# Kernel tuning notes

Measured on AMD Instinct MI355X. Metric: run time of the kernel, lower is better.

Reference implementation:

```python
import jax, jax.numpy as jnp
import numpy as np

B, C, D, H, W = 2, 96, 32, 64, 64
K = 2            # MRConv stride
EPS = 1e-5
SLOPE = 0.2      # LeakyReLU negative slope used by ViG act_layer('leakyrelu')


def conv1x1(x, w, b):
    # 1x1x1 Conv3d == per-voxel channel GEMM. x: [B,Ci,D,H,W], w: [Co,Ci]
    return jnp.einsum('bcdhw,oc->bodhw', x, w) + b[None, :, None, None, None]


def batchnorm(x, g, b):
    # training-mode BatchNorm3d: stats over (B, D, H, W)
    m = x.mean(axis=(0, 2, 3, 4), keepdims=True)
    v = x.var(axis=(0, 2, 3, 4), keepdims=True)
    return (x - m) * jax.lax.rsqrt(v + EPS) * g[None, :, None, None, None] + b[None, :, None, None, None]


def instnorm(x, g, b):
    # InstanceNorm3d: stats over (D, H, W) per sample/channel
    m = x.mean(axis=(2, 3, 4), keepdims=True)
    v = x.var(axis=(2, 3, 4), keepdims=True)
    return (x - m) * jax.lax.rsqrt(v + EPS) * g[None, :, None, None, None] + b[None, :, None, None, None]


def lrelu(x):
    return jnp.where(x >= 0, x, SLOPE * x)


def mr_aggregate(x):
    # MRConv shift/subtract/max, in closed form.
    # Original: x_j = max over axes a, shifts s in range(K, L_a, K) of (x - roll(x, s, a)), init 0.
    # Since shifts cover ALL nonzero multiples of K mod L_a (L_a % K == 0), the rolled values at a
    # position are exactly the other members of its residue class mod K along that axis, and
    # max(0, x - min_excluding_self) == x - min_including_self.  Hence:
    #   x_j = x - min over axes of (strided residue-class min along that axis).
    def axmin(x, axis):
        L = x.shape[axis]
        shp = list(x.shape)
        grp = shp[:axis] + [L // K, K] + shp[axis + 1:]
        xg = x.reshape(grp)
        m = xg.min(axis=axis, keepdims=True)             # min over same residue class
        return jnp.broadcast_to(m, grp).reshape(shp)
    m = jnp.minimum(jnp.minimum(axmin(x, 2), axmin(x, 3)), axmin(x, 4))
    return x - m


def setup_inputs() -> dict:
    key = jax.random.key(0)
    ks = jax.random.split(key, 8)
    f32 = jnp.float32
    def w(k, co, ci):
        return (jax.random.normal(k, (co, ci), dtype=f32) / np.sqrt(ci)).astype(f32)
    return {
        'x': jax.random.normal(ks[0], (B, C, D, H, W), dtype=f32),
        'w_fc1': w(ks[1], C, C), 'b_fc1': jnp.zeros((C,), f32),
        'g_bn1': jnp.ones((C,), f32), 'be_bn1': jnp.zeros((C,), f32),
        'w_g': w(ks[2], 2 * C, 2 * C), 'b_g': jnp.zeros((2 * C,), f32),
        'g_in': jnp.ones((2 * C,), f32), 'be_in': jnp.zeros((2 * C,), f32),
        'w_fc2': w(ks[3], C, 2 * C), 'b_fc2': jnp.zeros((C,), f32),
        'g_bn2': jnp.ones((C,), f32), 'be_bn2': jnp.zeros((C,), f32),
        'w_f1': w(ks[4], 4 * C, C), 'b_f1': jnp.zeros((4 * C,), f32),
        'g_bnf1': jnp.ones((4 * C,), f32), 'be_bnf1': jnp.zeros((4 * C,), f32),
        'w_f2': w(ks[5], C, 4 * C), 'b_f2': jnp.zeros((C,), f32),
        'g_bnf2': jnp.ones((C,), f32), 'be_bnf2': jnp.zeros((C,), f32),
    }


def reference(x, w_fc1, b_fc1, g_bn1, be_bn1, w_g, b_g, g_in, be_in,
              w_fc2, b_fc2, g_bn2, be_bn2, w_f1, b_f1, g_bnf1, be_bnf1,
              w_f2, b_f2, g_bnf2, be_bnf2):
    # ---- Grapher ----
    shortcut = x
    h = batchnorm(conv1x1(x, w_fc1, b_fc1), g_bn1, be_bn1)          # fc1: Conv+BN
    xj = mr_aggregate(h)                                            # MRConv shift-max agg
    hc = jnp.concatenate([h, xj], axis=1)                           # [B,2C,D,H,W]
    hg = lrelu(instnorm(conv1x1(hc, w_g, b_g), g_in, be_in))        # BasicConv: Conv+IN+LeakyReLU
    h = batchnorm(conv1x1(hg, w_fc2, b_fc2), g_bn2, be_bn2)         # fc2: Conv+BN
    x = h + shortcut
    # ---- FFN ----
    shortcut = x
    h = batchnorm(conv1x1(x, w_f1, b_f1), g_bnf1, be_bnf1)
    h = lrelu(h)
    h = batchnorm(conv1x1(h, w_f2, b_f2), g_bnf2, be_bnf2)
    return h + shortcut
```

## Files before the change

kernel.cpp:

```cpp
#include <hip/hip_runtime.h>
#include <hip/hip_bf16.h>


typedef __hip_bfloat16 bf16;
typedef __attribute__((ext_vector_type(8))) short short8;
typedef __attribute__((ext_vector_type(4))) float f4;
typedef __attribute__((ext_vector_type(2))) unsigned uint2v;

#define DEV static __device__ __forceinline__

constexpr int Sq  = 131072;
constexpr int NVq = 262144;

DEV float bu2f(unsigned short u) { return __uint_as_float(((unsigned)u) << 16); }
DEV unsigned short f2bu(float f) {
    unsigned i = __float_as_uint(f);
    unsigned r = i + 0x7FFFu + ((i >> 16) & 1u);
    return (unsigned short)(r >> 16);
}
DEV unsigned cvtpk(float a, float b) {
    unsigned r;
    asm("v_cvt_pk_bf16_f32 %0, %1, %2" : "=v"(r) : "v"(a), "v"(b));
    return r;
}
DEV void glds16(const void* g, void* l) {
    __builtin_amdgcn_global_load_lds(
        (const __attribute__((address_space(1))) unsigned*)g,
        (__attribute__((address_space(3))) unsigned*)l, 16, 0, 0);
}

template<int CIRB, int KP, int CO, int BN, int AMODE, bool PERB>
__global__ __launch_bounds__(256)
void conv_k(const char* __restrict__ A0, const char* __restrict__ A1,
            const char* __restrict__ Wb, const float* __restrict__ bias,
            const float* __restrict__ cfA, const float* __restrict__ cfB,
            bf16* __restrict__ Y, float* __restrict__ part)
{
    constexpr int NSTEP = KP / 64;
    constexpr int NF = BN / 16;
    constexpr int BI = BN / 8;
    __shared__ __align__(16) char smem[16384 + BN * 128];
    char* As = smem;
    char* Bs = smem + 16384;

    const int tid = threadIdx.x;
    const int lane = tid & 63, wid = tid >> 6, l16 = lane & 15, lhi = lane >> 4;
    const int gm = blockIdx.x, gy = blockIdx.y;
    const int v0 = gm * 128;
    const int b = gm >> 10;
    const int n0g = gy * BN;

    f4 acc[2][NF];
#pragma unroll
    for (int nf = 0; nf < NF; ++nf) {
        float bb = bias[n0g + nf * 16 + l16];
        f4 t = {bb, bb, bb, bb};
        acc[0][nf] = t; acc[1][nf] = t;
    }

    for (int s = 0; s < NSTEP; ++s) {
        for (int i = wid; i < BI; i += 4) {
            int o = i * 8 + (lane >> 3);
            glds16(Wb + (size_t)(n0g + o) * (KP * 2) + s * 128 + (((lane & 7) ^ (o & 7)) << 4),
                   Bs + i * 1024);
        }
        if constexpr (AMODE == 0) {
            for (int i = wid; i < 16; i += 4) {
                int r = i * 8 + (lane >> 3);
                glds16(A0 + (size_t)(v0 + r) * CIRB + s * 128 + (((lane & 7) ^ (r & 7)) << 4),
                       As + i * 1024);
            }
        } else {
#pragma unroll
            for (int j = 0; j < 4; ++j) {
                int idx = tid + 256 * j;
                int v = idx >> 3, u = idx & 7;
                int k8 = s * 8 + u;
                short8 hh;
                if constexpr (AMODE == 2) {
                    short8 raw = *(const short8*)(A0 + (size_t)(v0 + v) * CIRB + k8 * 16);
                    int cb = b * KP + k8 * 8;
                    f4 a0 = *(const f4*)(cfA + cb), a1 = *(const f4*)(cfA + cb + 4);
                    f4 d0 = *(const f4*)(cfB + cb), d1 = *(const f4*)(cfB + cb + 4);
#pragma unroll
                    for (int e = 0; e < 4; ++e) {
                        float t0 = fmaf(a0[e], bu2f((unsigned short)raw[e]),     d0[e]);
                        float t1 = fmaf(a1[e], bu2f((unsigned short)raw[e + 4]), d1[e]);
                        t0 = fmaxf(t0, 0.2f * t0);
                        t1 = fmaxf(t1, 0.2f * t1);
                        hh[e] = (short)f2bu(t0); hh[e + 4] = (short)f2bu(t1);
                    }
                } else {
                    if (k8 < 12) {
                        short8 raw = *(const short8*)(A0 + (size_t)(v0 + v) * 192 + k8 * 16);
                        int cb = k8 * 8;
                        f4 a0 = *(const f4*)(cfA + cb), a1 = *(const f4*)(cfA + cb + 4);
                        f4 d0 = *(const f4*)(cfB + cb), d1 = *(const f4*)(cfB + cb + 4);
#pragma unroll
                        for (int e = 0; e < 4; ++e) {
                            hh[e]     = (short)f2bu(fmaf(a0[e], bu2f((unsigned short)raw[e]),     d0[e]));
                            hh[e + 4] = (short)f2bu(fmaf(a1[e], bu2f((unsigned short)raw[e + 4]), d1[e]));
                        }
                    } else {
                        hh = *(const short8*)(A1 + (size_t)(v0 + v) * 192 + (k8 - 12) * 16);
                    }
                }
                *(short8*)(As + v * 128 + ((u ^ (v & 7)) << 4)) = hh;
            }
        }
        __syncthreads();
#pragma unroll
        for (int ks = 0; ks < 2; ++ks) {
            int kg = ks * 4 + lhi;
            short8 av[2];
#pragma unroll
            for (int mf = 0; mf < 2; ++mf) {
                int v = wid * 32 + mf * 16 + l16;
                av[mf] = *(const short8*)(As + v * 128 + ((kg ^ (v & 7)) << 4));
            }
#pragma unroll
            for (int nf = 0; nf < NF; ++nf) {
                int o = nf * 16 + l16;
                short8 bv = *(const short8*)(Bs + o * 128 + ((kg ^ (o & 7)) << 4));
                acc[0][nf] = __builtin_amdgcn_mfma_f32_16x16x32_bf16(av[0], bv, acc[0][nf], 0, 0, 0);
                acc[1][nf] = __builtin_amdgcn_mfma_f32_16x16x32_bf16(av[1], bv, acc[1][nf], 0, 0, 0);
            }
        }
        __syncthreads();
    }

#pragma unroll
    for (int mf = 0; mf < 2; ++mf) {
        int vb = v0 + wid * 32 + mf * 16 + lhi * 4;
#pragma unroll
        for (int nf = 0; nf < NF; ++nf) {
            int n = n0g + nf * 16 + l16;
#pragma unroll
            for (int r = 0; r < 4; ++r) {
                bf16 o; *(unsigned short*)&o = f2bu(acc[mf][nf][r]);
                Y[(size_t)(vb + r) * CO + n] = o;
            }
        }
    }
    float* ps = (float*)smem;
#pragma unroll
    for (int nf = 0; nf < NF; ++nf) {
        float sm = 0.f, sq = 0.f;
#pragma unroll
        for (int mf = 0; mf < 2; ++mf)
#pragma unroll
            for (int r = 0; r < 4; ++r) {
                float v = acc[mf][nf][r];
                sm += v; sq += v * v;
            }
        sm += __shfl_xor(sm, 16); sq += __shfl_xor(sq, 16);
        sm += __shfl_xor(sm, 32); sq += __shfl_xor(sq, 32);
        if (lane < 16) {
            ps[(wid * 2 + 0) * BN + nf * 16 + lane] = sm;
            ps[(wid * 2 + 1) * BN + nf * 16 + lane] = sq;
        }
    }
    __syncthreads();
    if (tid < BN) {
        float sm = ps[0 * BN + tid] + ps[2 * BN + tid] + ps[4 * BN + tid] + ps[6 * BN + tid];
        float sq = ps[1 * BN + tid] + ps[3 * BN + tid] + ps[5 * BN + tid] + ps[7 * BN + tid];
        int slot = PERB ? (b * 32 + (gm & 31)) : (gm & 63);
        float* pb = part + (size_t)(gy * 64 + slot) * 2 * BN;
        atomicAdd(&pb[tid], sm);
        atomicAdd(&pb[BN + tid], sq);
    }
}

__global__ __launch_bounds__(256)
void ffn_stats_k(const char* __restrict__ y2, const char* __restrict__ xT,
                 const float* __restrict__ cfA, const float* __restrict__ cfB,
                 const float* __restrict__ biasf1, const char* __restrict__ Wf1,
                 char* __restrict__ x2, float* __restrict__ part)
{
    __shared__ __align__(16) char Bs[96 * 192];
    __shared__ float ps[8 * 96];

    const int tid = threadIdx.x;
    const int lane = tid & 63, wid = tid >> 6, l16 = lane & 15, lhi = lane >> 4;
    const int gm = blockIdx.x;
    const int v0 = gm * 128;

    short8 afr[2][3];
#pragma unroll
    for (int mf = 0; mf < 2; ++mf)
#pragma unroll
        for (int ks = 0; ks < 3; ++ks) {
            int v = v0 + wid * 32 + mf * 16 + l16;
            int kg = ks * 4 + lhi, cb = kg * 8;
            short8 yv = *(const short8*)(y2 + (size_t)v * 192 + kg * 16);
            short8 xv = *(const short8*)(xT + (size_t)v * 192 + kg * 16);
            f4 a0 = *(const f4*)(cfA + cb), a1 = *(const f4*)(cfA + cb + 4);
            f4 d0 = *(const f4*)(cfB + cb), d1 = *(const f4*)(cfB + cb + 4);
            short8 o;
#pragma unroll
            for (int e = 0; e < 4; ++e) {
                float t0 = fmaf(a0[e], bu2f((unsigned short)yv[e]),     d0[e]) + bu2f((unsigned short)xv[e]);
                float t1 = fmaf(a1[e], bu2f((unsigned short)yv[e + 4]), d1[e]) + bu2f((unsigned short)xv[e + 4]);
                o[e]     = (short)f2bu(t0);
                o[e + 4] = (short)f2bu(t1);
            }
            afr[mf][ks] = o;
            *(short8*)(x2 + (size_t)v * 192 + kg * 16) = o;
        }

    for (int q = 0; q < 4; ++q) {
        for (int i = tid; i < 1152; i += 256) {
            int u = i / 96, o = i - u * 96;
            glds16(Wf1 + (size_t)(q * 96 + o) * 192 + (u << 4), Bs + (size_t)i * 16);
        }
        __syncthreads();
        f4 acc[2][6];
#pragma unroll
        for (int nf = 0; nf < 6; ++nf) {
            float bb = biasf1[q * 96 + nf * 16 + l16];
            f4 t = {bb, bb, bb, bb};
            acc[0][nf] = t; acc[1][nf] = t;
        }
#pragma unroll
        for (int ks = 0; ks < 3; ++ks) {
            int kg = ks * 4 + lhi;
#pragma unroll
            for (int nf = 0; nf < 6; ++nf) {
                int o = nf * 16 + l16;
                short8 bv = *(const short8*)(Bs + ((size_t)kg * 96 + o) * 16);
                acc[0][nf] = __builtin_amdgcn_mfma_f32_16x16x32_bf16(afr[0][ks], bv, acc[0][nf], 0, 0, 0);
                acc[1][nf] = __builtin_amdgcn_mfma_f32_16x16x32_bf16(afr[1][ks], bv, acc[1][nf], 0, 0, 0);
            }
        }
#pragma unroll
        for (int nf = 0; nf < 6; ++nf) {
            float sm = 0.f, sq = 0.f;
#pragma unroll
            for (int mf = 0; mf < 2; ++mf)
#pragma unroll
                for (int r = 0; r < 4; ++r) {
                    float v = acc[mf][nf][r];
                    sm += v; sq += v * v;
                }
            sm += __shfl_xor(sm, 16); sq += __shfl_xor(sq, 16);
            sm += __shfl_xor(sm, 32); sq += __shfl_xor(sq, 32);
            if (lane < 16) {
                ps[(wid * 2 + 0) * 96 + nf * 16 + lane] = sm;
                ps[(wid * 2 + 1) * 96 + nf * 16 + lane] = sq;
            }
        }
        __syncthreads();
        if (tid < 96) {
            float sm = ps[0 * 96 + tid] + ps[2 * 96 + tid] + ps[4 * 96 + tid] + ps[6 * 96 + tid];
            float sq = ps[1 * 96 + tid] + ps[3 * 96 + tid] + ps[5 * 96 + tid] + ps[7 * 96 + tid];
            float* pb = part + (size_t)(q * 64 + (gm & 63)) * 192;
            atomicAdd(&pb[tid], sm);
            atomicAdd(&pb[96 + tid], sq);
        }
        __syncthreads();
    }
}

__global__ __launch_bounds__(256)
void ffn_k(const char* __restrict__ x2, const float* __restrict__ cfA4,
           const float* __restrict__ cfB4, const float* __restrict__ biasf2,
           const char* __restrict__ Wf1, const char* __restrict__ Wf2,
           bf16* __restrict__ y4, float* __restrict__ part)
{
    __shared__ __align__(16) char W1c[12 * 64 * 16];
    __shared__ __align__(16) char W2c[8 * 96 * 16];
    __shared__ __align__(16) char zb[128 * 144];
    __shared__ float ps[8 * 96];

    const int tid = threadIdx.x;
    const int lane = tid & 63, wid = tid >> 6, l16 = lane & 15, lhi = lane >> 4;
    const int gm = blockIdx.x;
    const int v0 = gm * 128;

    short8 xfr[2][3];
#pragma unroll
    for (int nt = 0; nt < 2; ++nt)
#pragma unroll
        for (int ks = 0; ks < 3; ++ks)
            xfr[nt][ks] = *(const short8*)(x2 + (size_t)(v0 + wid * 32 + nt * 16 + l16) * 192
                                           + (ks * 4 + lhi) * 16);

    f4 accY[2][6];
#pragma unroll
    for (int nf = 0; nf < 6; ++nf) {
        float bb = biasf2[nf * 16 + l16];
        f4 t = {bb, bb, bb, bb};
        accY[0][nf] = t; accY[1][nf] = t;
    }

    for (int nc = 0; nc < 6; ++nc) {
        for (int i = tid; i < 768; i += 256) {
            int u = i / 64, o = i - u * 64;
            glds16(Wf1 + (size_t)(nc * 64 + o) * 192 + (u << 4), W1c + (size_t)i * 16);
        }
        for (int i = tid; i < 768; i += 256) {
            int u = i / 96, o = i - u * 96;
            glds16(Wf2 + (size_t)o * 768 + nc * 128 + (u << 4), W2c + (size_t)i * 16);
        }
        __syncthreads();

        f4 z[4][2];
#pragma unroll
        for (int mt = 0; mt < 4; ++mt) { z[mt][0] = f4{0,0,0,0}; z[mt][1] = f4{0,0,0,0}; }
#pragma unroll
        for (int ks = 0; ks < 3; ++ks) {
            int kg = ks * 4 + lhi;
#pragma unroll
            for (int mt = 0; mt < 4; ++mt) {
                int o = mt * 16 + l16;
                short8 wv = *(const short8*)(W1c + ((size_t)kg * 64 + o) * 16);
                z[mt][0] = __builtin_amdgcn_mfma_f32_16x16x32_bf16(wv, xfr[0][ks], z[mt][0], 0, 0, 0);
                z[mt][1] = __builtin_amdgcn_mfma_f32_16x16x32_bf16(wv, xfr[1][ks], z[mt][1], 0, 0, 0);
            }
        }
#pragma unroll
        for (int mt = 0; mt < 4; ++mt) {
            int ch = nc * 64 + mt * 16 + lhi * 4;
            f4 a = *(const f4*)(cfA4 + ch);
            f4 bb = *(const f4*)(cfB4 + ch);
#pragma unroll
            for (int nt = 0; nt < 2; ++nt) {
                int v = wid * 32 + nt * 16 + l16;
                float t0 = fmaf(a[0], z[mt][nt][0], bb[0]); t0 = fmaxf(t0, 0.2f * t0);
                float t1 = fmaf(a[1], z[mt][nt][1], bb[1]); t1 = fmaxf(t1, 0.2f * t1);
                float t2 = fmaf(a[2], z[mt][nt][2], bb[2]); t2 = fmaxf(t2, 0.2f * t2);
                float t3 = fmaf(a[3], z[mt][nt][3], bb[3]); t3 = fmaxf(t3, 0.2f * t3);
                uint2v w; w[0] = cvtpk(t0, t1); w[1] = cvtpk(t2, t3);
                *(uint2v*)(zb + (size_t)v * 144 + mt * 32 + lhi * 8) = w;
            }
        }
        asm volatile("s_waitcnt lgkmcnt(0)" ::: "memory");
        __builtin_amdgcn_sched_barrier(0);
#pragma unroll
        for (int ks = 0; ks < 2; ++ks) {
            int kg = ks * 4 + lhi;
            short8 av[2];
#pragma unroll
            for (int mf = 0; mf < 2; ++mf)
                av[mf] = *(const short8*)(zb + (size_t)(wid * 32 + mf * 16 + l16) * 144 + kg * 16);
#pragma unroll
            for (int nf = 0; nf < 6; ++nf) {
                int o = nf * 16 + l16;
                short8 bv = *(const short8*)(W2c + ((size_t)kg * 96 + o) * 16);
                accY[0][nf] = __builtin_amdgcn_mfma_f32_16x16x32_bf16(av[0], bv, accY[0][nf], 0, 0, 0);
                accY[1][nf] = __builtin_amdgcn_mfma_f32_16x16x32_bf16(av[1], bv, accY[1][nf], 0, 0, 0);
            }
        }
        __syncthreads();
    }

#pragma unroll
    for (int mf = 0; mf < 2; ++mf) {
        int vb = v0 + wid * 32 + mf * 16 + lhi * 4;
#pragma unroll
        for (int nf = 0; nf < 6; ++nf) {
            int n = nf * 16 + l16;
#pragma unroll
            for (int r = 0; r < 4; ++r) {
                bf16 o; *(unsigned short*)&o = f2bu(accY[mf][nf][r]);
                y4[(size_t)(vb + r) * 96 + n] = o;
            }
        }
    }
#pragma unroll
    for (int nf = 0; nf < 6; ++nf) {
        float sm = 0.f, sq = 0.f;
#pragma unroll
        for (int mf = 0; mf < 2; ++mf)
#pragma unroll
            for (int r = 0; r < 4; ++r) {
                float v = accY[mf][nf][r];
                sm += v; sq += v * v;
            }
        sm += __shfl_xor(sm, 16); sq += __shfl_xor(sq, 16);
        sm += __shfl_xor(sm, 32); sq += __shfl_xor(sq, 32);
        if (lane < 16) {
            ps[(wid * 2 + 0) * 96 + nf * 16 + lane] = sm;
            ps[(wid * 2 + 1) * 96 + nf * 16 + lane] = sq;
        }
    }
    __syncthreads();
    if (tid < 96) {
        float sm = ps[0 * 96 + tid] + ps[2 * 96 + tid] + ps[4 * 96 + tid] + ps[6 * 96 + tid];
        float sq = ps[1 * 96 + tid] + ps[3 * 96 + tid] + ps[5 * 96 + tid] + ps[7 * 96 + tid];
        float* pb = part + (size_t)(gm & 63) * 192;
        atomicAdd(&pb[tid], sm);
        atomicAdd(&pb[96 + tid], sq);
    }
}

__global__ void finalize_k(const float* __restrict__ part, float* __restrict__ cf,
                           const float* __restrict__ g, const float* __restrict__ be,
                           const float* __restrict__ bias,
                           int nStats, int CO, int BN, int perB, float invN)
{
    int s = blockIdx.x * 64 + threadIdx.x;
    if (s >= nStats) return;
    int ch = perB ? (s % CO) : s;
    int bb = perB ? (s / CO) : 0;
    int gy = ch / BN, c = ch - gy * BN;
    int j0 = perB ? bb * 32 : 0, cnt = perB ? 32 : 64;
    float sm = 0.f, sq = 0.f;
    for (int j = 0; j < cnt; ++j) {
        const float* pb = part + (size_t)(gy * 64 + j0 + j) * 2 * BN;
        sm += pb[c]; sq += pb[BN + c];
    }
    float m = sm * invN;
    float var = fmaf(-m, m, sq * invN);
    float A = g[ch] * rsqrtf(var + 1e-5f);
    cf[s] = A;
    float B = fmaf(-m, A, be[ch]);
    if (bias) B = fmaf(A, bias[ch], B);
    cf[1024 + s] = B;
}

__global__ void wprep_k(const float* __restrict__ w0, const float* __restrict__ w1,
                        const float* __restrict__ w2, const float* __restrict__ w3,
                        const float* __restrict__ w4, bf16* __restrict__ Wb)
{
    int i = blockIdx.x * 256 + threadIdx.x;
    if (i >= 141312) return;
    const float* src; int r, KP, CI, off;
    if (i < 12288)       { src = w0; r = i;          KP = 128; CI = 96;  off = 0; }
    else if (i < 49152)  { src = w1; r = i - 12288;  KP = 192; CI = 192; off = 12288; }
    else if (i < 67584)  { src = w2; r = i - 49152;  KP = 192; CI = 192; off = 49152; }
    else if (i < 104448) { src = w3; r = i - 67584;  KP = 96;  CI = 96;  off = 67584; }
    else                 { src = w4; r = i - 104448; KP = 384; CI = 384; off = 104448; }
    int o = r / KP, k = r - o * KP;
    float v = (k < CI) ? src[o * CI + k] : 0.f;
    bf16 h; *(unsigned short*)&h = f2bu(v);
    Wb[off + r] = h;
}

__global__ __launch_bounds__(256)
void tin_k(const float* __restrict__ x, char* __restrict__ xT)
{
    __shared__ float ldsT[128 * 97];
    const int gm = blockIdx.x, b = gm >> 10, s0 = (gm & 1023) * 128;
    const int t = threadIdx.x;
#pragma unroll
    for (int i = 0; i < 12; ++i) {
        int idx = t + 256 * i;
        int c = idx >> 5, s4 = idx & 31;
        f4 r = *(const f4*)(x + ((size_t)(b * 96 + c) << 17) + s0 + s4 * 4);
#pragma unroll
        for (int j = 0; j < 4; ++j) ldsT[(s4 * 4 + j) * 97 + c] = r[j];
    }
    __syncthreads();
#pragma unroll
    for (int i = 0; i < 6; ++i) {
        int idx = t + 256 * i;
        int r = idx / 12, uc = idx % 12, cb = uc * 8;
        short8 o;
#pragma unroll
        for (int e = 0; e < 8; ++e) o[e] = (short)f2bu(ldsT[r * 97 + cb + e]);
        *(short8*)(xT + (size_t)(b * Sq + s0 + r) * 192 + uc * 16) = o;
    }
}

__global__ __launch_bounds__(192)
void mr_dmin_k(const char* __restrict__ y1, char* __restrict__ dminp)
{
    const int wq = blockIdx.x >> 1, dh = blockIdx.x & 1;
    const int h = blockIdx.y, b = blockIdx.z;
    const int t = threadIdx.x;
    const int w = wq * 16 + t / 12, uc = t % 12;
    const char* base = y1 + (size_t)(b * Sq + dh * 16 * 4096 + h * 64 + w) * 192 + uc * 16;
    float mn[2][8];
#pragma unroll
    for (int p = 0; p < 2; ++p)
#pragma unroll
        for (int e = 0; e < 8; ++e) mn[p][e] = 1e30f;
#pragma unroll 4
    for (int i = 0; i < 16; ++i) {
        short8 raw = *(const short8*)(base + (size_t)i * (4096 * 192));
        int p = i & 1;
#pragma unroll
        for (int e = 0; e < 8; ++e)
            mn[p][e] = fminf(mn[p][e], bu2f((unsigned short)raw[e]));
    }
#pragma unroll
    for (int p = 0; p < 2; ++p) {
        short8 o;
#pragma unroll
        for (int e = 0; e < 8; ++e) o[e] = (short)f2bu(mn[p][e]);
        *(short8*)(dminp + (size_t)((((b * 64 + h) * 64 + w) * 2 + dh) * 2 + p) * 192 + uc * 16) = o;
    }
}

__global__ __launch_bounds__(192)
void mr_hmin_k(const char* __restrict__ y1, char* __restrict__ hminp)
{
    const int wq = blockIdx.x >> 2, hq = blockIdx.x & 3;
    const int d = blockIdx.y, b = blockIdx.z;
    const int t = threadIdx.x;
    const int w = wq * 16 + t / 12, uc = t % 12;
    const char* base = y1 + (size_t)(b * Sq + d * 4096 + hq * 16 * 64 + w) * 192 + uc * 16;
    float mn[2][8];
#pragma unroll
    for (int p = 0; p < 2; ++p)
#pragma unroll
        for (int e = 0; e < 8; ++e) mn[p][e] = 1e30f;
#pragma unroll 4
    for (int i = 0; i < 16; ++i) {
        short8 raw = *(const short8*)(base + (size_t)i * (64 * 192));
        int p = i & 1;
#pragma unroll
        for (int e = 0; e < 8; ++e)
            mn[p][e] = fminf(mn[p][e], bu2f((unsigned short)raw[e]));
    }
#pragma unroll
    for (int p = 0; p < 2; ++p) {
        short8 o;
#pragma unroll
        for (int e = 0; e < 8; ++e) o[e] = (short)f2bu(mn[p][e]);
        *(short8*)(hminp + (size_t)((((b * 32 + d) * 64 + w) * 4 + hq) * 2 + p) * 192 + uc * 16) = o;
    }
}

__global__ __launch_bounds__(256)
void mr_p2_k(const char* __restrict__ y1, const float* __restrict__ cfA,
             const char* __restrict__ dminp, const char* __restrict__ hminp,
             char* __restrict__ xj)
{
    __shared__ __align__(16) char rowb[64 * 96 * 2];
    __shared__ float wlds[2 * 96];
    const int h = blockIdx.x, d = blockIdx.y, b = blockIdx.z;
    const int t = threadIdx.x;

    short8 hv[3];
#pragma unroll
    for (int j = 0; j < 3; ++j) {
        int slot = t + 256 * j;
        int w = slot / 12, uc = slot % 12;
        short8 raw = *(const short8*)(y1 + (size_t)(b * Sq + d * 4096 + h * 64 + w) * 192 + uc * 16);
        hv[j] = raw;
        *(short8*)(rowb + slot * 16) = raw;
    }
    __syncthreads();
    if (t < 192) {
        int p = t / 96, c = t % 96;
        float m = 1e30f;
        for (int w2 = p; w2 < 64; w2 += 2)
            m = fminf(m, bu2f(*(const unsigned short*)(rowb + (w2 * 96 + c) * 2)));
        wlds[t] = m;
    }
    __syncthreads();
#pragma unroll
    for (int j = 0; j < 3; ++j) {
        int slot = t + 256 * j;
        int w = slot / 12, uc = slot % 12, cb = uc * 8;
        const char* dp = dminp + (size_t)((((b * 64 + h) * 64 + w) * 2) * 2 + (d & 1)) * 192 + uc * 16;
        short8 dm0 = *(const short8*)(dp);
        short8 dm1 = *(const short8*)(dp + 384);
        const char* hp = hminp + (size_t)((((b * 32 + d) * 64 + w) * 4) * 2 + (h & 1)) * 192 + uc * 16;
        short8 hm0 = *(const short8*)(hp);
        short8 hm1 = *(const short8*)(hp + 384);
        short8 hm2 = *(const short8*)(hp + 768);
        short8 hm3 = *(const short8*)(hp + 1152);
        f4 a0 = *(const f4*)(cfA + cb), a1 = *(const f4*)(cfA + cb + 4);
        short8 xo;
#pragma unroll
        for (int e = 0; e < 8; ++e) {
            float m = fminf(
                fminf(bu2f((unsigned short)dm0[e]), bu2f((unsigned short)dm1[e])),
                fminf(fminf(fminf(bu2f((unsigned short)hm0[e]), bu2f((unsigned short)hm1[e])),
                            fminf(bu2f((unsigned short)hm2[e]), bu2f((unsigned short)hm3[e]))),
                      wlds[(w & 1) * 96 + cb + e]));
            float A = (e < 4) ? a0[e] : a1[e - 4];
            xo[e] = (short)f2bu(A * (bu2f((unsigned short)hv[j][e]) - m));
        }
        *(short8*)(xj + (size_t)(b * Sq + d * 4096 + h * 64 + w) * 192 + uc * 16) = xo;
    }
}

__global__ __launch_bounds__(256)
void tout_k(const char* __restrict__ y4, const float* __restrict__ cfA,
            const float* __restrict__ cfB, const char* __restrict__ x2,
            float* __restrict__ outp)
{
    __shared__ float ldsT[128 * 97];
    const int gm = blockIdx.x, b = gm >> 10, s0 = (gm & 1023) * 128;
    const int t = threadIdx.x;
#pragma unroll
    for (int i = 0; i < 6; ++i) {
        int idx = t + 256 * i;
        int r = idx / 12, uc = idx % 12, cb = uc * 8;
        size_t vv = (size_t)(b * Sq + s0 + r);
        short8 yv = *(const short8*)(y4 + vv * 192 + uc * 16);
        short8 xv = *(const short8*)(x2 + vv * 192 + uc * 16);
        f4 a0 = *(const f4*)(cfA + cb), a1 = *(const f4*)(cfA + cb + 4);
        f4 d0 = *(const f4*)(cfB + cb), d1 = *(const f4*)(cfB + cb + 4);
#pragma unroll
        for (int e = 0; e < 4; ++e) {
            ldsT[r * 97 + cb + e]     = fmaf(a0[e], bu2f((unsigned short)yv[e]),     d0[e]) + bu2f((unsigned short)xv[e]);
            ldsT[r * 97 + cb + e + 4] = fmaf(a1[e], bu2f((unsigned short)yv[e + 4]), d1[e]) + bu2f((unsigned short)xv[e + 4]);
        }
    }
    __syncthreads();
#pragma unroll
    for (int i = 0; i < 12; ++i) {
        int idx = t + 256 * i;
        int c = idx >> 5, s4 = idx & 31;
        f4 o;
#pragma unroll
        for (int j = 0; j < 4; ++j) o[j] = ldsT[(s4 * 4 + j) * 97 + c];
        *(f4*)(outp + ((size_t)(b * 96 + c) << 17) + s0 + s4 * 4) = o;
    }
}

extern "C" void kernel_launch(void* const* d_in, const int* in_sizes, int n_in,
                              void* d_out, int out_size, void* d_ws, size_t ws_size,
                              hipStream_t stream)
{
    (void)in_sizes; (void)n_in; (void)out_size; (void)ws_size;

    const float* x      = (const float*)d_in[0];
    const float* w_fc1  = (const float*)d_in[1];
    const float* b_fc1  = (const float*)d_in[2];
    const float* g_bn1  = (const float*)d_in[3];
    const float* be_bn1 = (const float*)d_in[4];
    const float* w_g    = (const float*)d_in[5];
    const float* b_g    = (const float*)d_in[6];
    const float* g_in   = (const float*)d_in[7];
    const float* be_in  = (const float*)d_in[8];
    const float* w_fc2  = (const float*)d_in[9];
    const float* b_fc2  = (const float*)d_in[10];
    const float* g_bn2  = (const float*)d_in[11];
    const float* be_bn2 = (const float*)d_in[12];
    const float* w_f1   = (const float*)d_in[13];
    const float* b_f1   = (const float*)d_in[14];
    const float* g_bnf1 = (const float*)d_in[15];
    const float* be_bnf1= (const float*)d_in[16];
    const float* w_f2   = (const float*)d_in[17];
    const float* b_f2   = (const float*)d_in[18];
    const float* g_bnf2 = (const float*)d_in[19];
    const float* be_bnf2= (const float*)d_in[20];
    float* outp = (float*)d_out;

    char* W = (char*)d_ws;
    char* xT    = W;
    char* y1    = W + 50331648ull;
    char* dminp = W + 100663296ull;
    char* hminp = W + 113246208ull;
    char* xj    = W + 125829120ull;
    char* yg    = W + 176160768ull;
    char* y2    = W + 50331648ull;
    char* y4    = W + 201326592ull;
    char* x2    = W + 251658240ull;
    char* M     = W + 301989888ull;
    bf16*  Wb   = (bf16*)M;
    float* cf   = (float*)(M + 307200);
    float* part = (float*)(M + 348160);

    hipMemsetAsync(part, 0, 5 * 196608, stream);

    const float invBN = 1.f / (float)NVq, invIN = 1.f / (float)Sq;
    dim3 blk(256);
    float* c1 = cf, *c2 = cf + 2048, *c3 = cf + 4096, *c4 = cf + 6144, *c5 = cf + 8192;
    const char* Wfc1 = (const char*)Wb;
    const char* Wg   = (const char*)Wb + 24576;
    const char* Wfc2 = (const char*)Wb + 98304;
    const char* Wf1  = (const char*)Wb + 135168;
    const char* Wf2  = (const char*)Wb + 208896;

    wprep_k<<<552, blk, 0, stream>>>(w_fc1, w_g, w_fc2, w_f1, w_f2, Wb);
    tin_k<<<2048, blk, 0, stream>>>(x, xT);

    conv_k<192, 128, 96, 96, 0, false><<<dim3(2048, 1), blk, 0, stream>>>(
        xT, nullptr, Wfc1, b_fc1, nullptr, nullptr, (bf16*)y1, part);
    finalize_k<<<2, 64, 0, stream>>>(part, c1, g_bn1, be_bn1, nullptr, 96, 96, 96, 0, invBN);

    mr_dmin_k<<<dim3(8, 64, 2), dim3(192), 0, stream>>>(y1, dminp);
    mr_hmin_k<<<dim3(16, 32, 2), dim3(192), 0, stream>>>(y1, hminp);
    mr_p2_k<<<dim3(64, 32, 2), blk, 0, stream>>>(y1, c1, dminp, hminp, xj);

    conv_k<192, 192, 192, 192, 4, true><<<dim3(2048, 1), blk, 0, stream>>>(
        y1, xj, Wg, b_g, c1, c1 + 1024, (bf16*)yg, part + 49152);
    finalize_k<<<6, 64, 0, stream>>>(part + 49152, c2, g_in, be_in, nullptr, 384, 192, 192, 1, invIN);

    conv_k<384, 192, 96, 96, 2, false><<<dim3(2048, 1), blk, 0, stream>>>(
        yg, nullptr, Wfc2, b_fc2, c2, c2 + 1024, (bf16*)y2, part + 98304);
    finalize_k<<<2, 64, 0, stream>>>(part + 98304, c3, g_bn2, be_bn2, nullptr, 96, 96, 96, 0, invBN);

    ffn_stats_k<<<2048, blk, 0, stream>>>(y2, xT, c3, c3 + 1024, b_f1, Wf1, x2, part + 147456);
    finalize_k<<<6, 64, 0, stream>>>(part + 147456, c4, g_bnf1, be_bnf1, b_f1, 384, 384, 96, 0, invBN);

    ffn_k<<<2048, blk, 0, stream>>>(x2, c4, c4 + 1024, b_f2, Wf1, Wf2, (bf16*)y4, part + 196608);
    finalize_k<<<2, 64, 0, stream>>>(part + 196608, c5, g_bnf2, be_bnf2, nullptr, 96, 96, 96, 0, invBN);

    tout_k<<<2048, blk, 0, stream>>>(y4, c5, c5 + 1024, x2, outp);
}
```

Before: 458.8 us.

## Recompute grapher conv in fused kernel instead of materializing its output

The 192-channel grapher conv output (yg) is no longer written to memory. A stats-only pass computes instance-norm statistics, and a second fused kernel recomputes the conv, applies instnorm+LeakyReLU in registers, and feeds the fc2 GEMM directly through LDS. This removes the write and re-read of a large bf16 intermediate in exchange for doing the grapher GEMM twice. conv_k is simplified to the only remaining mode.

```diff
diff --git a/kernel.cpp b/kernel.cpp
--- a/kernel.cpp
+++ b/kernel.cpp
@@ -29,12 +29,11 @@
         (__attribute__((address_space(3))) unsigned*)l, 16, 0, 0);
 }
 
-template<int CIRB, int KP, int CO, int BN, int AMODE, bool PERB>
+template<int CIRB, int KP, int CO, int BN>
 __global__ __launch_bounds__(256)
-void conv_k(const char* __restrict__ A0, const char* __restrict__ A1,
-            const char* __restrict__ Wb, const float* __restrict__ bias,
-            const float* __restrict__ cfA, const float* __restrict__ cfB,
-            bf16* __restrict__ Y, float* __restrict__ part)
+void conv_k(const char* __restrict__ A0, const char* __restrict__ Wb,
+            const float* __restrict__ bias, bf16* __restrict__ Y,
+            float* __restrict__ part)
 {
     constexpr int NSTEP = KP / 64;
     constexpr int NF = BN / 16;
@@ -45,15 +44,13 @@
 
     const int tid = threadIdx.x;
     const int lane = tid & 63, wid = tid >> 6, l16 = lane & 15, lhi = lane >> 4;
-    const int gm = blockIdx.x, gy = blockIdx.y;
+    const int gm = blockIdx.x;
     const int v0 = gm * 128;
-    const int b = gm >> 10;
-    const int n0g = gy * BN;
 
     f4 acc[2][NF];
 #pragma unroll
     for (int nf = 0; nf < NF; ++nf) {
-        float bb = bias[n0g + nf * 16 + l16];
+        float bb = bias[nf * 16 + l16];
         f4 t = {bb, bb, bb, bb};
         acc[0][nf] = t; acc[1][nf] = t;
     }
@@ -61,52 +58,13 @@
     for (int s = 0; s < NSTEP; ++s) {
         for (int i = wid; i < BI; i += 4) {
             int o = i * 8 + (lane >> 3);
-            glds16(Wb + (size_t)(n0g + o) * (KP * 2) + s * 128 + (((lane & 7) ^ (o & 7)) << 4),
+            glds16(Wb + (size_t)o * (KP * 2) + s * 128 + (((lane & 7) ^ (o & 7)) << 4),
                    Bs + i * 1024);
         }
-        if constexpr (AMODE == 0) {
-            for (int i = wid; i < 16; i += 4) {
-                int r = i * 8 + (lane >> 3);
-                glds16(A0 + (size_t)(v0 + r) * CIRB + s * 128 + (((lane & 7) ^ (r & 7)) << 4),
-                       As + i * 1024);
-            }
-        } else {
-#pragma unroll
-            for (int j = 0; j < 4; ++j) {
-                int idx = tid + 256 * j;
-                int v = idx >> 3, u = idx & 7;
-                int k8 = s * 8 + u;
-                short8 hh;
-                if constexpr (AMODE == 2) {
-                    short8 raw = *(const short8*)(A0 + (size_t)(v0 + v) * CIRB + k8 * 16);
-                    int cb = b * KP + k8 * 8;
-                    f4 a0 = *(const f4*)(cfA + cb), a1 = *(const f4*)(cfA + cb + 4);
-                    f4 d0 = *(const f4*)(cfB + cb), d1 = *(const f4*)(cfB + cb + 4);
-#pragma unroll
-                    for (int e = 0; e < 4; ++e) {
-                        float t0 = fmaf(a0[e], bu2f((unsigned short)raw[e]),     d0[e]);
-                        float t1 = fmaf(a1[e], bu2f((unsigned short)raw[e + 4]), d1[e]);
-                        t0 = fmaxf(t0, 0.2f * t0);
-                        t1 = fmaxf(t1, 0.2f * t1);
-                        hh[e] = (short)f2bu(t0); hh[e + 4] = (short)f2bu(t1);
-                    }
-                } else {
-                    if (k8 < 12) {
-                        short8 raw = *(const short8*)(A0 + (size_t)(v0 + v) * 192 + k8 * 16);
-                        int cb = k8 * 8;
-                        f4 a0 = *(const f4*)(cfA + cb), a1 = *(const f4*)(cfA + cb + 4);
-                        f4 d0 = *(const f4*)(cfB + cb), d1 = *(const f4*)(cfB + cb + 4);
-#pragma unroll
-                        for (int e = 0; e < 4; ++e) {
-                            hh[e]     = (short)f2bu(fmaf(a0[e], bu2f((unsigned short)raw[e]),     d0[e]));
-                            hh[e + 4] = (short)f2bu(fmaf(a1[e], bu2f((unsigned short)raw[e + 4]), d1[e]));
-                        }
-                    } else {
-                        hh = *(const short8*)(A1 + (size_t)(v0 + v) * 192 + (k8 - 12) * 16);
-                    }
-                }
-                *(short8*)(As + v * 128 + ((u ^ (v & 7)) << 4)) = hh;
-            }
+        for (int i = wid; i < 16; i += 4) {
+            int r = i * 8 + (lane >> 3);
+            glds16(A0 + (size_t)(v0 + r) * CIRB + s * 128 + (((lane & 7) ^ (r & 7)) << 4),
+                   As + i * 1024);
         }
         __syncthreads();
 #pragma unroll
@@ -134,7 +92,7 @@
         int vb = v0 + wid * 32 + mf * 16 + lhi * 4;
 #pragma unroll
         for (int nf = 0; nf < NF; ++nf) {
-            int n = n0g + nf * 16 + l16;
+            int n = nf * 16 + l16;
 #pragma unroll
             for (int r = 0; r < 4; ++r) {
                 bf16 o; *(unsigned short*)&o = f2bu(acc[mf][nf][r]);
@@ -164,10 +122,217 @@
     if (tid < BN) {
         float sm = ps[0 * BN + tid] + ps[2 * BN + tid] + ps[4 * BN + tid] + ps[6 * BN + tid];
         float sq = ps[1 * BN + tid] + ps[3 * BN + tid] + ps[5 * BN + tid] + ps[7 * BN + tid];
-        int slot = PERB ? (b * 32 + (gm & 31)) : (gm & 63);
-        float* pb = part + (size_t)(gy * 64 + slot) * 2 * BN;
+        float* pb = part + (size_t)(gm & 63) * 2 * BN;
         atomicAdd(&pb[tid], sm);
         atomicAdd(&pb[BN + tid], sq);
+    }
+}
+
+DEV short8 load_hx(const char* __restrict__ y1, const char* __restrict__ xj,
+                   const float* __restrict__ cA, const float* __restrict__ cB,
+                   size_t v, int k8)
+{
+    if (k8 < 12) {
+        short8 raw = *(const short8*)(y1 + v * 192 + k8 * 16);
+        int cb = k8 * 8;
+        f4 a0 = *(const f4*)(cA + cb), a1 = *(const f4*)(cA + cb + 4);
+        f4 d0 = *(const f4*)(cB + cb), d1 = *(const f4*)(cB + cb + 4);
+        short8 hh;
+#pragma unroll
+        for (int e = 0; e < 4; ++e) {
+            hh[e]     = (short)f2bu(fmaf(a0[e], bu2f((unsigned short)raw[e]),     d0[e]));
+            hh[e + 4] = (short)f2bu(fmaf(a1[e], bu2f((unsigned short)raw[e + 4]), d1[e]));
+        }
+        return hh;
+    }
+    return *(const short8*)(xj + v * 192 + (k8 - 12) * 16);
+}
+
+__global__ __launch_bounds__(256)
+void g_stats_k(const char* __restrict__ y1, const char* __restrict__ xj,
+               const float* __restrict__ c1A, const float* __restrict__ c1B,
+               const float* __restrict__ biasg, const char* __restrict__ Wg,
+               float* __restrict__ part)
+{
+    __shared__ __align__(16) char W1c[24 * 64 * 16];
+    __shared__ float ps[4 * 2 * 192];
+
+    const int tid = threadIdx.x;
+    const int lane = tid & 63, wid = tid >> 6, l16 = lane & 15, lhi = lane >> 4;
+    const int gm = blockIdx.x;
+    const int v0 = gm * 64;
+
+    short8 hfr[6];
+#pragma unroll
+    for (int ks = 0; ks < 6; ++ks)
+        hfr[ks] = load_hx(y1, xj, c1A, c1B, (size_t)(v0 + wid * 16 + l16), ks * 4 + lhi);
+
+    for (int nc = 0; nc < 3; ++nc) {
+        for (int i = tid; i < 1536; i += 256) {
+            int u = i >> 6, o = i & 63;
+            glds16(Wg + (size_t)(nc * 64 + o) * 384 + (u << 4), W1c + (size_t)i * 16);
+        }
+        __syncthreads();
+        f4 z[4];
+#pragma unroll
+        for (int mt = 0; mt < 4; ++mt)
+            z[mt] = *(const f4*)(biasg + nc * 64 + mt * 16 + lhi * 4);
+#pragma unroll
+        for (int ks = 0; ks < 6; ++ks) {
+            int kg = ks * 4 + lhi;
+#pragma unroll
+            for (int mt = 0; mt < 4; ++mt) {
+                short8 wv = *(const short8*)(W1c + ((size_t)kg * 64 + mt * 16 + l16) * 16);
+                z[mt] = __builtin_amdgcn_mfma_f32_16x16x32_bf16(wv, hfr[ks], z[mt], 0, 0, 0);
+            }
+        }
+#pragma unroll
+        for (int mt = 0; mt < 4; ++mt) {
+            f4 sv, qv;
+#pragma unroll
+            for (int r = 0; r < 4; ++r) {
+                float sm = z[mt][r], sq = sm * sm;
+                sm += __shfl_xor(sm, 1); sq += __shfl_xor(sq, 1);
+                sm += __shfl_xor(sm, 2); sq += __shfl_xor(sq, 2);
+                sm += __shfl_xor(sm, 4); sq += __shfl_xor(sq, 4);
+                sm += __shfl_xor(sm, 8); sq += __shfl_xor(sq, 8);
+                sv[r] = sm; qv[r] = sq;
+            }
+            if (l16 == 0) {
+                int ch = nc * 64 + mt * 16 + lhi * 4;
+                *(f4*)&ps[(wid * 2 + 0) * 192 + ch] = sv;
+                *(f4*)&ps[(wid * 2 + 1) * 192 + ch] = qv;
+            }
+        }
+        __syncthreads();
+    }
+    if (tid < 192) {
+        float sm = ps[0 * 192 + tid] + ps[2 * 192 + tid] + ps[4 * 192 + tid] + ps[6 * 192 + tid];
+        float sq = ps[1 * 192 + tid] + ps[3 * 192 + tid] + ps[5 * 192 + tid] + ps[7 * 192 + tid];
+        int slot = (gm >> 11) * 32 + (gm & 31);
+        float* pb = part + (size_t)slot * 2 * 192;
+        atomicAdd(&pb[tid], sm);
+        atomicAdd(&pb[192 + tid], sq);
+    }
+}
+
+__global__ __launch_bounds__(256)
+void g_fused_k(const char* __restrict__ y1, const char* __restrict__ xj,
+               const float* __restrict__ c1A, const float* __restrict__ c1B,
+               const float* __restrict__ c2A, const float* __restrict__ c2B,
+               const float* __restrict__ biasg, const float* __restrict__ biasfc2,
+               const char* __restrict__ Wg, const char* __restrict__ Wfc2,
+               bf16* __restrict__ y2, float* __restrict__ part)
+{
+    __shared__ __align__(16) char W1c[24 * 64 * 16];
+    __shared__ __align__(16) char W2c[96 * 8 * 16];
+    __shared__ __align__(16) char zb[64 * 144];
+    __shared__ float ps[4 * 2 * 96];
+
+    const int tid = threadIdx.x;
+    const int lane = tid & 63, wid = tid >> 6, l16 = lane & 15, lhi = lane >> 4;
+    const int gm = blockIdx.x;
+    const int v0 = gm * 64;
+    const int b = gm >> 11;
+
+    short8 hfr[6];
+#pragma unroll
+    for (int ks = 0; ks < 6; ++ks)
+        hfr[ks] = load_hx(y1, xj, c1A, c1B, (size_t)(v0 + wid * 16 + l16), ks * 4 + lhi);
+
+    f4 accY[6];
+#pragma unroll
+    for (int nf = 0; nf < 6; ++nf) {
+        float bb = biasfc2[nf * 16 + l16];
+        accY[nf] = f4{bb, bb, bb, bb};
+    }
+
+    for (int nc = 0; nc < 3; ++nc) {
+        for (int i = tid; i < 1536; i += 256) {
+            int u = i >> 6, o = i & 63;
+            glds16(Wg + (size_t)(nc * 64 + o) * 384 + (u << 4), W1c + (size_t)i * 16);
+        }
+        for (int i = tid; i < 768; i += 256) {
+            int o = i >> 3, s = i & 7;
+            glds16(Wfc2 + (size_t)o * 384 + nc * 128 + ((s ^ (o & 7)) << 4),
+                   W2c + (size_t)i * 16);
+        }
+        __syncthreads();
+
+        f4 z[4];
+#pragma unroll
+        for (int mt = 0; mt < 4; ++mt)
+            z[mt] = *(const f4*)(biasg + nc * 64 + mt * 16 + lhi * 4);
+#pragma unroll
+        for (int ks = 0; ks < 6; ++ks) {
+            int kg = ks * 4 + lhi;
+#pragma unroll
+            for (int mt = 0; mt < 4; ++mt) {
+                short8 wv = *(const short8*)(W1c + ((size_t)kg * 64 + mt * 16 + l16) * 16);
+                z[mt] = __builtin_amdgcn_mfma_f32_16x16x32_bf16(wv, hfr[ks], z[mt], 0, 0, 0);
+            }
+        }
+#pragma unroll
+        for (int mt = 0; mt < 4; ++mt) {
+            int ch = b * 192 + nc * 64 + mt * 16 + lhi * 4;
+            f4 a = *(const f4*)(c2A + ch);
+            f4 bb = *(const f4*)(c2B + ch);
+            int v = wid * 16 + l16;
+            float t0 = fmaf(a[0], z[mt][0], bb[0]); t0 = fmaxf(t0, 0.2f * t0);
+            float t1 = fmaf(a[1], z[mt][1], bb[1]); t1 = fmaxf(t1, 0.2f * t1);
+            float t2 = fmaf(a[2], z[mt][2], bb[2]); t2 = fmaxf(t2, 0.2f * t2);
+            float t3 = fmaf(a[3], z[mt][3], bb[3]); t3 = fmaxf(t3, 0.2f * t3);
+            uint2v w; w[0] = cvtpk(t0, t1); w[1] = cvtpk(t2, t3);
+            *(uint2v*)(zb + (size_t)v * 144 + mt * 32 + lhi * 8) = w;
+        }
+        asm volatile("s_waitcnt lgkmcnt(0)" ::: "memory");
+        __builtin_amdgcn_sched_barrier(0);
+#pragma unroll
+        for (int ks = 0; ks < 2; ++ks) {
+            int kg = ks * 4 + lhi;
+            short8 av = *(const short8*)(zb + (size_t)(wid * 16 + l16) * 144 + kg * 16);
+#pragma unroll
+            for (int nf = 0; nf < 6; ++nf) {
+                int o = nf * 16 + l16;
+                short8 bv = *(const short8*)(W2c + ((size_t)o * 8 + (kg ^ (o & 7))) * 16);
+                accY[nf] = __builtin_amdgcn_mfma_f32_16x16x32_bf16(av, bv, accY[nf], 0, 0, 0);
+            }
+        }
+        __syncthreads();
+    }
+
+    const int vb = v0 + wid * 16 + lhi * 4;
+#pragma unroll
+    for (int nf = 0; nf < 6; ++nf) {
+        int n = nf * 16 + l16;
+#pragma unroll
+        for (int r = 0; r < 4; ++r) {
+            bf16 o; *(unsigned short*)&o = f2bu(accY[nf][r]);
+            y2[(size_t)(vb + r) * 96 + n] = o;
+        }
+    }
+#pragma unroll
+    for (int nf = 0; nf < 6; ++nf) {
+        float sm = 0.f, sq = 0.f;
+#pragma unroll
+        for (int r = 0; r < 4; ++r) {
+            float v = accY[nf][r];
+            sm += v; sq += v * v;
+        }
+        sm += __shfl_xor(sm, 16); sq += __shfl_xor(sq, 16);
+        sm += __shfl_xor(sm, 32); sq += __shfl_xor(sq, 32);
+        if (lane < 16) {
+            ps[(wid * 2 + 0) * 96 + nf * 16 + lane] = sm;
+            ps[(wid * 2 + 1) * 96 + nf * 16 + lane] = sq;
+        }
+    }
+    __syncthreads();
+    if (tid < 96) {
+        float sm = ps[0 * 96 + tid] + ps[2 * 96 + tid] + ps[4 * 96 + tid] + ps[6 * 96 + tid];
+        float sq = ps[1 * 96 + tid] + ps[3 * 96 + tid] + ps[5 * 96 + tid] + ps[7 * 96 + tid];
+        float* pb = part + (size_t)(gm & 63) * 2 * 96;
+        atomicAdd(&pb[tid], sm);
+        atomicAdd(&pb[96 + tid], sq);
     }
 }
 
@@ -649,8 +814,7 @@
     char* dminp = W + 100663296ull;
     char* hminp = W + 113246208ull;
     char* xj    = W + 125829120ull;
-    char* yg    = W + 176160768ull;
-    char* y2    = W + 50331648ull;
+    char* y2    = W + 176160768ull;
     char* y4    = W + 201326592ull;
     char* x2    = W + 251658240ull;
     char* M     = W + 301989888ull;
@@ -672,20 +836,19 @@
     wprep_k<<<552, blk, 0, stream>>>(w_fc1, w_g, w_fc2, w_f1, w_f2, Wb);
     tin_k<<<2048, blk, 0, stream>>>(x, xT);
 
-    conv_k<192, 128, 96, 96, 0, false><<<dim3(2048, 1), blk, 0, stream>>>(
-        xT, nullptr, Wfc1, b_fc1, nullptr, nullptr, (bf16*)y1, part);
+    conv_k<192, 128, 96, 96><<<2048, blk, 0, stream>>>(
+        xT, Wfc1, b_fc1, (bf16*)y1, part);
     finalize_k<<<2, 64, 0, stream>>>(part, c1, g_bn1, be_bn1, nullptr, 96, 96, 96, 0, invBN);
 
     mr_dmin_k<<<dim3(8, 64, 2), dim3(192), 0, stream>>>(y1, dminp);
     mr_hmin_k<<<dim3(16, 32, 2), dim3(192), 0, stream>>>(y1, hminp);
     mr_p2_k<<<dim3(64, 32, 2), blk, 0, stream>>>(y1, c1, dminp, hminp, xj);
 
-    conv_k<192, 192, 192, 192, 4, true><<<dim3(2048, 1), blk, 0, stream>>>(
-        y1, xj, Wg, b_g, c1, c1 + 1024, (bf16*)yg, part + 49152);
+    g_stats_k<<<4096, blk, 0, stream>>>(y1, xj, c1, c1 + 1024, b_g, Wg, part + 49152);
     finalize_k<<<6, 64, 0, stream>>>(part + 49152, c2, g_in, be_in, nullptr, 384, 192, 192, 1, invIN);
 
-    conv_k<384, 192, 96, 96, 2, false><<<dim3(2048, 1), blk, 0, stream>>>(
-        yg, nullptr, Wfc2, b_fc2, c2, c2 + 1024, (bf16*)y2, part + 98304);
+    g_fused_k<<<4096, blk, 0, stream>>>(y1, xj, c1, c1 + 1024, c2, c2 + 1024,
+                                        b_g, b_fc2, Wg, Wfc2, (bf16*)y2, part + 98304);
     finalize_k<<<2, 64, 0, stream>>>(part + 98304, c3, g_bn2, be_bn2, nullptr, 96, 96, 96, 0, invBN);
 
     ffn_stats_k<<<2048, blk, 0, stream>>>(y2, xT, c3, c3 + 1024, b_f1, Wf1, x2, part + 147456);
```

Result: slower. 536.2 us (+16.9%).
